# Optimization experiments

Hardware: AMD Instinct MI355X
Metric: run time of the kernel (lower is better)

The kernel has to match this reference:

```python
import jax, jax.numpy as jnp
import numpy as np
from jax import lax

N_EXPERTS = 16
TOP_K = 2
D_MODEL = 512
D_FF = 2048


def setup_inputs() -> dict:
    key = jax.random.key(0)
    ks = jax.random.split(key, 7)
    s_in = 1.0 / np.sqrt(D_MODEL)
    s_ff = 1.0 / np.sqrt(D_FF)
    x = jax.random.normal(ks[0], (2, 2048, D_MODEL), dtype=jnp.float32)
    router_w = jax.random.uniform(ks[1], (N_EXPERTS, D_MODEL), jnp.float32, -s_in, s_in)
    router_b = jax.random.uniform(ks[2], (N_EXPERTS,), jnp.float32, -s_in, s_in)
    w1 = jax.random.uniform(ks[3], (N_EXPERTS, D_FF, D_MODEL), jnp.float32, -s_in, s_in)
    b1 = jax.random.uniform(ks[4], (N_EXPERTS, D_FF), jnp.float32, -s_in, s_in)
    w2 = jax.random.uniform(ks[5], (N_EXPERTS, D_MODEL, D_FF), jnp.float32, -s_ff, s_ff)
    b2 = jax.random.uniform(ks[6], (N_EXPERTS, D_MODEL), jnp.float32, -s_ff, s_ff)
    return {"x": x, "router_w": router_w, "router_b": router_b,
            "w1": w1, "b1": b1, "w2": w2, "b2": b2}


def reference(x, router_w, router_b, w1, b1, w2, b2):
    B, S, D = x.shape
    xt = x.reshape(-1, D)                                   # [T, D]
    logits = xt @ router_w.T + router_b                     # [T, E]
    probs = jax.nn.softmax(logits, axis=-1)
    topk_p, topk_i = lax.top_k(probs, TOP_K)                # [T, K]
    # Dense gate matrix: gate[t, e] = topk prob if expert e selected else 0.
    # Weighting by gate reproduces the masked gather/scatter-add exactly.
    onehot = jax.nn.one_hot(topk_i, N_EXPERTS, dtype=probs.dtype)  # [T, K, E]
    gates = jnp.sum(onehot * topk_p[..., None], axis=1)     # [T, E]

    def expert_step(acc, packed):
        w1e, b1e, w2e, b2e, ge = packed                     # per-expert params + gate col [T]
        h = jax.nn.gelu(xt @ w1e.T + b1e, approximate=False)  # [T, D_FF]
        y = h @ w2e.T + b2e                                 # [T, D]
        return acc + y * ge[:, None], None

    out, _ = lax.scan(expert_step, jnp.zeros_like(xt),
                      (w1, b1, w2, b2, gates.T))
    return out.reshape(B, S, D)
```

## Files before the change

### kernel.cpp

```cpp
#include <hip/hip_runtime.h>
#include <stdint.h>

#define T_TOK 4096
#define DM    512
#define DFF   2048
#define NE    16
#define NSLOT (T_TOK * 2)
#define NW    (NE * DFF * DM)
#define MAXTILE 80
#define CONVB (2 * NW / 8 / 256)
#define ROUTB (T_TOK / 4)
#define KSPLIT 4

typedef __attribute__((ext_vector_type(8))) short  bf16x8;
typedef __attribute__((ext_vector_type(4))) float  f32x4;
typedef __attribute__((ext_vector_type(8))) unsigned short us8;

static __device__ __forceinline__ unsigned short f2bf(float f) {
    unsigned int u = __float_as_uint(f);
    u += 0x7FFFu + ((u >> 16) & 1u);
    return (unsigned short)(u >> 16);
}

static __device__ __forceinline__ void gload_lds16(const void* g, void* l) {
    __builtin_amdgcn_global_load_lds(
        (const __attribute__((address_space(1))) void*)g,
        (__attribute__((address_space(3))) void*)l, 16, 0, 0);
}

static __device__ __forceinline__ int xcd_chunk_logical(int bid, int total) {
    int k = bid & 7, seq = bid >> 3;
    int q = total >> 3, r = total & 7;
    int base = k * q + (k < r ? k : r);
    int len  = q + (k < r ? 1 : 0);
    return (seq < len) ? (base + seq) : total;
}

__global__ __launch_bounds__(256) void convert_router_kernel(
    const float* __restrict__ w1, const float* __restrict__ w2,
    unsigned short* __restrict__ w1b, unsigned short* __restrict__ w2b,
    const float* __restrict__ x, const float* __restrict__ rw,
    const float* __restrict__ rb, int* __restrict__ tok_e,
    float* __restrict__ tok_g, unsigned short* __restrict__ xb,
    const float* __restrict__ b2, float* __restrict__ out)
{
    __shared__ float rws[NE * DM];
    int tid = threadIdx.x;

    if (blockIdx.x >= ROUTB) {
        size_t i = ((size_t)(blockIdx.x - ROUTB) * 256 + tid) * 8;
        const float* src; unsigned short* dst;
        if (i < (size_t)NW) { src = w1 + i;        dst = w1b + i; }
        else                { src = w2 + (i - NW); dst = w2b + (i - NW); }
        f32x4 a = __builtin_nontemporal_load((const f32x4*)src);
        f32x4 b = __builtin_nontemporal_load((const f32x4*)(src + 4));
        us8 v;
        v[0] = f2bf(a.x); v[1] = f2bf(a.y); v[2] = f2bf(a.z); v[3] = f2bf(a.w);
        v[4] = f2bf(b.x); v[5] = f2bf(b.y); v[6] = f2bf(b.z); v[7] = f2bf(b.w);
        *(us8*)dst = v;
        return;
    }

    for (int i = 0; i < 8; ++i) {
        int idx = (tid + i * 256) * 4;
        *(f32x4*)&rws[idx] = *(const f32x4*)&rw[idx];
    }
    __syncthreads();

    int wid = tid >> 6, lane = tid & 63;
    int t = blockIdx.x * 4 + wid;

    float xv[8];
    const float* xp = x + (size_t)t * DM + lane * 8;
    *(f32x4*)&xv[0] = *(const f32x4*)xp;
    *(f32x4*)&xv[4] = *(const f32x4*)(xp + 4);

    us8 v;
    for (int i = 0; i < 8; ++i) v[i] = f2bf(xv[i]);
    *(us8*)&xb[(size_t)t * DM + lane * 8] = v;

    float acc[NE];
    for (int e = 0; e < NE; ++e) {
        const float* wp = &rws[e * DM + lane * 8];
        float a = 0.f;
        for (int i = 0; i < 8; ++i) a += xv[i] * wp[i];
        acc[e] = a;
    }
    for (int e = 0; e < NE; ++e) {
        float v2 = acc[e];
        for (int off = 32; off > 0; off >>= 1) v2 += __shfl_xor(v2, off);
        acc[e] = v2 + rb[e];
    }
    float m = acc[0];
    for (int e = 1; e < NE; ++e) m = fmaxf(m, acc[e]);
    float p[NE]; float s = 0.f;
    for (int e = 0; e < NE; ++e) { p[e] = expf(acc[e] - m); s += p[e]; }
    float inv = 1.f / s;
    int i0 = 0; float p0 = p[0];
    for (int e = 1; e < NE; ++e) if (p[e] > p0) { p0 = p[e]; i0 = e; }
    int i1 = (i0 == 0) ? 1 : 0; float p1 = p[i1];
    for (int e = 0; e < NE; ++e)
        if (e != i0 && p[e] > p1) { p1 = p[e]; i1 = e; }
    float g0 = p0 * inv, g1 = p1 * inv;
    if (lane == 0) {
        tok_e[t * 2]     = i0;  tok_e[t * 2 + 1] = i1;
        tok_g[t * 2]     = g0;
        tok_g[t * 2 + 1] = g1;
    }
    {
        int d = lane * 8;
        f32x4 c0a = *(const f32x4*)&b2[i0 * DM + d];
        f32x4 c0b = *(const f32x4*)&b2[i0 * DM + d + 4];
        f32x4 c1a = *(const f32x4*)&b2[i1 * DM + d];
        f32x4 c1b = *(const f32x4*)&b2[i1 * DM + d + 4];
        f32x4 oa, ob;
        for (int i = 0; i < 4; ++i) {
            oa[i] = g0 * c0a[i] + g1 * c1a[i];
            ob[i] = g0 * c0b[i] + g1 * c1b[i];
        }
        *(f32x4*)&out[(size_t)t * DM + d]     = oa;
        *(f32x4*)&out[(size_t)t * DM + d + 4] = ob;
    }
}

__global__ __launch_bounds__(1024) void compact_kernel(
    const int* __restrict__ tok_e, const float* __restrict__ tok_g,
    int* __restrict__ slot_token, float* __restrict__ slot_gate,
    int* __restrict__ eoff)
{
    __shared__ int wsum[16][NE];
    __shared__ int wbase[16][NE];
    __shared__ int ebl[NE];
    int tid = threadIdx.x;
    int wv = tid >> 6, lane = tid & 63;

    int ent[8];
    *(int4*)&ent[0] = *(const int4*)&tok_e[tid * 8];
    *(int4*)&ent[4] = *(const int4*)&tok_e[tid * 8 + 4];
    float gv[8];
    *(f32x4*)&gv[0] = *(const f32x4*)&tok_g[tid * 8];
    *(f32x4*)&gv[4] = *(const f32x4*)&tok_g[tid * 8 + 4];

    int cnt[NE], isc[NE];
#pragma unroll
    for (int e = 0; e < NE; ++e) {
        int c = 0;
#pragma unroll
        for (int i = 0; i < 8; ++i) c += (ent[i] == e) ? 1 : 0;
        int v = c;
#pragma unroll
        for (int off = 1; off < 64; off <<= 1) {
            int u = __shfl_up(v, off);
            if (lane >= off) v += u;
        }
        cnt[e] = c; isc[e] = v;
    }
    if (lane == 63) {
#pragma unroll
        for (int e = 0; e < NE; ++e) wsum[wv][e] = isc[e];
    }
    __syncthreads();
    if (wv == 0 && lane < NE) {
        int e = lane, s = 0;
#pragma unroll
        for (int w = 0; w < 16; ++w) { wbase[w][e] = s; s += wsum[w][e]; }
        int til = (s + 127) >> 7;
        int rs = s, rt = til;
#pragma unroll
        for (int off = 1; off < 16; off <<= 1) {
            int u1 = __shfl_up(rs, off);
            int u2 = __shfl_up(rt, off);
            if (lane >= off) { rs += u1; rt += u2; }
        }
        ebl[e] = rs - s;
        eoff[e] = rs - s;
        eoff[16 + e] = s;
        eoff[32 + e] = rt - til;
        if (e == NE - 1) eoff[48] = rt;
    }
    __syncthreads();
    int ofs[NE];
#pragma unroll
    for (int e = 0; e < NE; ++e)
        ofs[e] = ebl[e] + wbase[wv][e] + isc[e] - cnt[e];
#pragma unroll
    for (int i = 0; i < 8; ++i) {
        int ei = ent[i], s = 0;
#pragma unroll
        for (int e = 0; e < NE; ++e) if (ei == e) s = ofs[e];
        slot_token[s] = tid * 4 + (i >> 1);
        slot_gate[s]  = gv[i];
#pragma unroll
        for (int e = 0; e < NE; ++e) if (ei == e) ofs[e] = s + 1;
    }
}

__global__ __launch_bounds__(256) void gemm1_kernel(
    const unsigned short* __restrict__ xb, const unsigned short* __restrict__ w1b,
    const float* __restrict__ b1, const int* __restrict__ slot_token,
    const int* __restrict__ eoff, unsigned short* __restrict__ h)
{
    __shared__ unsigned short smem[16384];
    __shared__ int tokrow[128];
    __shared__ int meta[49];
    unsigned short* As = smem;
    unsigned short* Bs = smem + 8192;

    int tid = threadIdx.x;
    if (tid < 49) meta[tid] = eoff[tid];
    __syncthreads();

    int lg = xcd_chunk_logical(blockIdx.x, meta[48] * 16);
    int slot_idx = lg >> 4;
    if (slot_idx >= meta[48]) return;
    int nB = (lg & 15) * 128;
    int e = 0;
    while (e < NE - 1 && meta[32 + e + 1] <= slot_idx) ++e;
    int mt  = slot_idx - meta[32 + e];
    int off = meta[e], cnt = meta[16 + e];
    int slot0 = off + mt * 128;
    int valid = cnt - mt * 128; if (valid > 128) valid = 128;

    if (tid < 128) {
        int s = slot0 + tid; if (s > NSLOT - 1) s = NSLOT - 1;
        tokrow[tid] = slot_token[s];
    }
    __syncthreads();

    f32x4 acc[16];
    for (int i = 0; i < 16; ++i) acc[i] = (f32x4){0.f, 0.f, 0.f, 0.f};

    const unsigned short* wb = w1b + ((size_t)e * DFF + nB) * DM;
    int wid = tid >> 6, l = tid & 63;
    int wm = (wid & 1) * 64, wn = (wid >> 1) * 64;
    int q = l >> 4, c = l & 15;

    for (int kt = 0; kt < DM / 64; ++kt) {
        for (int j = 0; j < 4; ++j) {
            int u = (wid * 4 + j) * 64 + l;
            int row = u >> 3, sc = (u & 7) ^ (row & 7);
            gload_lds16(xb + (size_t)tokrow[row] * DM + kt * 64 + sc * 8, &As[u * 8]);
        }
        for (int j = 0; j < 4; ++j) {
            int u = (wid * 4 + j) * 64 + l;
            int row = u >> 3, sc = (u & 7) ^ (row & 7);
            gload_lds16(wb + (size_t)row * DM + kt * 64 + sc * 8, &Bs[u * 8]);
        }
        __syncthreads();
        for (int ks = 0; ks < 2; ++ks) {
            int sw = ((ks * 4 + q) ^ (c & 7)) * 8;
            bf16x8 af[4], bv[4];
            for (int i = 0; i < 4; ++i) af[i] = *(bf16x8*)&As[(wm + i * 16 + c) * 64 + sw];
            for (int j = 0; j < 4; ++j) bv[j] = *(bf16x8*)&Bs[(wn + j * 16 + c) * 64 + sw];
            for (int i = 0; i < 4; ++i)
                for (int j = 0; j < 4; ++j)
                    acc[i * 4 + j] = __builtin_amdgcn_mfma_f32_16x16x32_bf16(
                        af[i], bv[j], acc[i * 4 + j], 0, 0, 0);
        }
        __syncthreads();
    }

    float bias[4];
    for (int j = 0; j < 4; ++j) bias[j] = b1[e * DFF + nB + wn + j * 16 + c];
    unsigned short* bounce = smem;
    for (int ph = 0; ph < 2; ++ph) {
        __syncthreads();
        if ((wid & 1) == ph) {
            for (int i = 0; i < 4; ++i)
                for (int j = 0; j < 4; ++j) {
                    f32x4 a = acc[i * 4 + j];
                    for (int r = 0; r < 4; ++r) {
                        int rl = i * 16 + q * 4 + r;
                        float z = a[r] + bias[j];
                        float u2 = z * fmaf(0.0356774081f, z * z, 0.7978845608f);
                        float ex = __expf(2.0f * u2);
                        float th = 1.0f - 2.0f * __builtin_amdgcn_rcpf(ex + 1.0f);
                        float g = 0.5f * z * (1.0f + th);
                        bounce[rl * 136 + wn + j * 16 + c] = f2bf(g);
                    }
                }
        }
        __syncthreads();
        for (int it = 0; it < 4; ++it) {
            int u2 = it * 256 + tid;
            int row = u2 >> 4, ch = u2 & 15;
            int gr = ph * 64 + row;
            if (gr < valid)
                *(us8*)&h[(size_t)(slot0 + gr) * DFF + nB + ch * 8] =
                    *(us8*)&bounce[row * 136 + ch * 8];
        }
    }
}

__global__ __launch_bounds__(256) void gemm2_kernel(
    const unsigned short* __restrict__ h, const unsigned short* __restrict__ w2b,
    const int* __restrict__ eoff, const int* __restrict__ slot_token,
    const float* __restrict__ slot_gate, float* __restrict__ out)
{
    __shared__ unsigned short smem[16384];
    __shared__ int meta[49];
    __shared__ int tokrow[128];
    __shared__ float sgate[128];
    unsigned short* As = smem;
    unsigned short* Bs = smem + 8192;

    int tid = threadIdx.x;
    if (tid < 49) meta[tid] = eoff[tid];
    __syncthreads();

    int lg = xcd_chunk_logical(blockIdx.x, meta[48] * 16);
    int slot_idx = lg >> 4;
    if (slot_idx >= meta[48]) return;
    int nB = (lg & 3) * 128;
    int z  = (lg >> 2) & 3;
    int e = 0;
    while (e < NE - 1 && meta[32 + e + 1] <= slot_idx) ++e;
    int mt  = slot_idx - meta[32 + e];
    int off = meta[e], cnt = meta[16 + e];
    int slot0 = off + mt * 128;
    int valid = cnt - mt * 128; if (valid > 128) valid = 128;

    if (tid < 128) {
        int s = slot0 + tid; if (s > NSLOT - 1) s = NSLOT - 1;
        tokrow[tid] = slot_token[s];
        sgate[tid]  = slot_gate[s];
    }
    __syncthreads();

    f32x4 acc[16];
    for (int i = 0; i < 16; ++i) acc[i] = (f32x4){0.f, 0.f, 0.f, 0.f};

    const unsigned short* wb = w2b + ((size_t)e * DM + nB) * DFF
                             + (size_t)z * (DFF / KSPLIT);
    const unsigned short* hz = h + (size_t)z * (DFF / KSPLIT);
    int wid = tid >> 6, l = tid & 63;
    int wm = (wid & 1) * 64, wn = (wid >> 1) * 64;
    int q = l >> 4, c = l & 15;

    for (int kt = 0; kt < DFF / (64 * KSPLIT); ++kt) {
        for (int j = 0; j < 4; ++j) {
            int u = (wid * 4 + j) * 64 + l;
            int row = u >> 3, sc = (u & 7) ^ (row & 7);
            size_t s = slot0 + row; if (s > NSLOT - 1) s = NSLOT - 1;
            gload_lds16(hz + s * DFF + kt * 64 + sc * 8, &As[u * 8]);
        }
        for (int j = 0; j < 4; ++j) {
            int u = (wid * 4 + j) * 64 + l;
            int row = u >> 3, sc = (u & 7) ^ (row & 7);
            gload_lds16(wb + (size_t)row * DFF + kt * 64 + sc * 8, &Bs[u * 8]);
        }
        __syncthreads();
        for (int ks = 0; ks < 2; ++ks) {
            int sw = ((ks * 4 + q) ^ (c & 7)) * 8;
            bf16x8 af[4], bv[4];
            for (int i = 0; i < 4; ++i) af[i] = *(bf16x8*)&As[(wm + i * 16 + c) * 64 + sw];
            for (int j = 0; j < 4; ++j) bv[j] = *(bf16x8*)&Bs[(wn + j * 16 + c) * 64 + sw];
            for (int i = 0; i < 4; ++i)
                for (int j = 0; j < 4; ++j)
                    acc[i * 4 + j] = __builtin_amdgcn_mfma_f32_16x16x32_bf16(
                        af[i], bv[j], acc[i * 4 + j], 0, 0, 0);
        }
        __syncthreads();
    }

    for (int i = 0; i < 4; ++i)
        for (int j = 0; j < 4; ++j) {
            int n = nB + wn + j * 16 + c;
            for (int r = 0; r < 4; ++r) {
                int rl = wm + i * 16 + q * 4 + r;
                if (rl < valid)
                    atomicAdd(&out[(size_t)tokrow[rl] * DM + n],
                              sgate[rl] * acc[i * 4 + j][r]);
            }
        }
}

extern "C" void kernel_launch(void* const* d_in, const int* in_sizes, int n_in,
                              void* d_out, int out_size, void* d_ws, size_t ws_size,
                              hipStream_t stream) {
    const float* x  = (const float*)d_in[0];
    const float* rw = (const float*)d_in[1];
    const float* rb = (const float*)d_in[2];
    const float* w1 = (const float*)d_in[3];
    const float* b1 = (const float*)d_in[4];
    const float* w2 = (const float*)d_in[5];
    const float* b2 = (const float*)d_in[6];
    float* out = (float*)d_out;

    char* ws = (char*)d_ws;
    size_t o = 0;
    unsigned short* h   = (unsigned short*)(ws + o); o += (size_t)NSLOT * DFF * 2;
    unsigned short* w1b = (unsigned short*)(ws + o); o += (size_t)NW * 2;
    unsigned short* w2b = (unsigned short*)(ws + o); o += (size_t)NW * 2;
    unsigned short* xb  = (unsigned short*)(ws + o); o += (size_t)T_TOK * DM * 2;
    int*   tok_e      = (int*)(ws + o);   o += (size_t)NSLOT * 4;
    float* tok_g      = (float*)(ws + o); o += (size_t)NSLOT * 4;
    int*   slot_token = (int*)(ws + o);   o += (size_t)NSLOT * 4;
    float* slot_gate  = (float*)(ws + o); o += (size_t)NSLOT * 4;
    int*   eoff       = (int*)(ws + o);

    convert_router_kernel<<<ROUTB + CONVB, 256, 0, stream>>>(
        w1, w2, w1b, w2b, x, rw, rb, tok_e, tok_g, xb, b2, out);
    compact_kernel<<<1, 1024, 0, stream>>>(
        tok_e, tok_g, slot_token, slot_gate, eoff);
    gemm1_kernel<<<16 * MAXTILE, 256, 0, stream>>>(
        xb, w1b, b1, slot_token, eoff, h);
    gemm2_kernel<<<4 * MAXTILE * KSPLIT, 256, 0, stream>>>(
        h, w2b, eoff, slot_token, slot_gate, out);
}
```

Baseline: 304.2 us.

## Replace gemm2 atomic scatter with per-split slot buffers and a combine kernel

The second GEMM now writes plain, non-atomic partial outputs per slot into two K-split buffers, which reuse the w1 bf16 workspace after gemm1 finishes. A new combine kernel then gathers each token's two slots, adds both K-split partials and the expert bias, applies the gates, and writes the output once. KSPLIT drops from 4 to 2, so gemm2 launches fewer but longer blocks. This removes scattered float atomics and the bias pre-initialisation in the router, at the cost of an extra kernel launch and extra memory traffic for the intermediate y buffers.

```diff
diff --git a/kernel.cpp b/kernel.cpp
--- a/kernel.cpp
+++ b/kernel.cpp
@@ -6,11 +6,11 @@
 #define DFF   2048
 #define NE    16
 #define NSLOT (T_TOK * 2)
-#define NW    (NE * DFF * DM)
+#define NW    (16 * 2048 * 512)
 #define MAXTILE 80
 #define CONVB (2 * NW / 8 / 256)
 #define ROUTB (T_TOK / 4)
-#define KSPLIT 4
+#define KSPLIT 2
 
 typedef __attribute__((ext_vector_type(8))) short  bf16x8;
 typedef __attribute__((ext_vector_type(4))) float  f32x4;
@@ -41,8 +41,7 @@
     unsigned short* __restrict__ w1b, unsigned short* __restrict__ w2b,
     const float* __restrict__ x, const float* __restrict__ rw,
     const float* __restrict__ rb, int* __restrict__ tok_e,
-    float* __restrict__ tok_g, unsigned short* __restrict__ xb,
-    const float* __restrict__ b2, float* __restrict__ out)
+    float* __restrict__ tok_g, unsigned short* __restrict__ xb)
 {
     __shared__ float rws[NE * DM];
     int tid = threadIdx.x;
@@ -101,32 +100,16 @@
     int i1 = (i0 == 0) ? 1 : 0; float p1 = p[i1];
     for (int e = 0; e < NE; ++e)
         if (e != i0 && p[e] > p1) { p1 = p[e]; i1 = e; }
-    float g0 = p0 * inv, g1 = p1 * inv;
     if (lane == 0) {
         tok_e[t * 2]     = i0;  tok_e[t * 2 + 1] = i1;
-        tok_g[t * 2]     = g0;
-        tok_g[t * 2 + 1] = g1;
-    }
-    {
-        int d = lane * 8;
-        f32x4 c0a = *(const f32x4*)&b2[i0 * DM + d];
-        f32x4 c0b = *(const f32x4*)&b2[i0 * DM + d + 4];
-        f32x4 c1a = *(const f32x4*)&b2[i1 * DM + d];
-        f32x4 c1b = *(const f32x4*)&b2[i1 * DM + d + 4];
-        f32x4 oa, ob;
-        for (int i = 0; i < 4; ++i) {
-            oa[i] = g0 * c0a[i] + g1 * c1a[i];
-            ob[i] = g0 * c0b[i] + g1 * c1b[i];
-        }
-        *(f32x4*)&out[(size_t)t * DM + d]     = oa;
-        *(f32x4*)&out[(size_t)t * DM + d + 4] = ob;
+        tok_g[t * 2]     = p0 * inv;
+        tok_g[t * 2 + 1] = p1 * inv;
     }
 }
 
 __global__ __launch_bounds__(1024) void compact_kernel(
-    const int* __restrict__ tok_e, const float* __restrict__ tok_g,
-    int* __restrict__ slot_token, float* __restrict__ slot_gate,
-    int* __restrict__ eoff)
+    const int* __restrict__ tok_e, int* __restrict__ slot_token,
+    int* __restrict__ tok_slot, int* __restrict__ eoff)
 {
     __shared__ int wsum[16][NE];
     __shared__ int wbase[16][NE];
@@ -137,9 +120,6 @@
     int ent[8];
     *(int4*)&ent[0] = *(const int4*)&tok_e[tid * 8];
     *(int4*)&ent[4] = *(const int4*)&tok_e[tid * 8 + 4];
-    float gv[8];
-    *(f32x4*)&gv[0] = *(const f32x4*)&tok_g[tid * 8];
-    *(f32x4*)&gv[4] = *(const f32x4*)&tok_g[tid * 8 + 4];
 
     int cnt[NE], isc[NE];
 #pragma unroll
@@ -189,7 +169,7 @@
 #pragma unroll
         for (int e = 0; e < NE; ++e) if (ei == e) s = ofs[e];
         slot_token[s] = tid * 4 + (i >> 1);
-        slot_gate[s]  = gv[i];
+        tok_slot[tid * 8 + i] = s;
 #pragma unroll
         for (int e = 0; e < NE; ++e) if (ei == e) ofs[e] = s + 1;
     }
@@ -294,13 +274,10 @@
 
 __global__ __launch_bounds__(256) void gemm2_kernel(
     const unsigned short* __restrict__ h, const unsigned short* __restrict__ w2b,
-    const int* __restrict__ eoff, const int* __restrict__ slot_token,
-    const float* __restrict__ slot_gate, float* __restrict__ out)
+    const int* __restrict__ eoff, float* __restrict__ y)
 {
     __shared__ unsigned short smem[16384];
     __shared__ int meta[49];
-    __shared__ int tokrow[128];
-    __shared__ float sgate[128];
     unsigned short* As = smem;
     unsigned short* Bs = smem + 8192;
 
@@ -308,24 +285,17 @@
     if (tid < 49) meta[tid] = eoff[tid];
     __syncthreads();
 
-    int lg = xcd_chunk_logical(blockIdx.x, meta[48] * 16);
-    int slot_idx = lg >> 4;
+    int lg = xcd_chunk_logical(blockIdx.x, meta[48] * 8);
+    int slot_idx = lg >> 3;
     if (slot_idx >= meta[48]) return;
     int nB = (lg & 3) * 128;
-    int z  = (lg >> 2) & 3;
+    int z  = (lg >> 2) & 1;
     int e = 0;
     while (e < NE - 1 && meta[32 + e + 1] <= slot_idx) ++e;
     int mt  = slot_idx - meta[32 + e];
     int off = meta[e], cnt = meta[16 + e];
     int slot0 = off + mt * 128;
     int valid = cnt - mt * 128; if (valid > 128) valid = 128;
-
-    if (tid < 128) {
-        int s = slot0 + tid; if (s > NSLOT - 1) s = NSLOT - 1;
-        tokrow[tid] = slot_token[s];
-        sgate[tid]  = slot_gate[s];
-    }
-    __syncthreads();
 
     f32x4 acc[16];
     for (int i = 0; i < 16; ++i) acc[i] = (f32x4){0.f, 0.f, 0.f, 0.f};
@@ -363,16 +333,40 @@
         __syncthreads();
     }
 
+    float* yz = y + (size_t)z * NSLOT * DM;
     for (int i = 0; i < 4; ++i)
         for (int j = 0; j < 4; ++j) {
             int n = nB + wn + j * 16 + c;
             for (int r = 0; r < 4; ++r) {
                 int rl = wm + i * 16 + q * 4 + r;
                 if (rl < valid)
-                    atomicAdd(&out[(size_t)tokrow[rl] * DM + n],
-                              sgate[rl] * acc[i * 4 + j][r]);
+                    yz[(size_t)(slot0 + rl) * DM + n] = acc[i * 4 + j][r];
             }
         }
+}
+
+__global__ __launch_bounds__(256) void combine_kernel(
+    const float* __restrict__ y, const float* __restrict__ b2,
+    const int* __restrict__ tok_slot, const float* __restrict__ tok_g,
+    const int* __restrict__ tok_e, float* __restrict__ out)
+{
+    int tid = threadIdx.x;
+    int t = blockIdx.x * 2 + (tid >> 7);
+    int d = (tid & 127) * 4;
+    int s0 = tok_slot[t * 2], s1 = tok_slot[t * 2 + 1];
+    float g0 = tok_g[t * 2], g1 = tok_g[t * 2 + 1];
+    int e0 = tok_e[t * 2], e1 = tok_e[t * 2 + 1];
+    const float* yB = y + (size_t)NSLOT * DM;
+    f32x4 y0a = *(const f32x4*)&y [(size_t)s0 * DM + d];
+    f32x4 y0b = *(const f32x4*)&yB[(size_t)s0 * DM + d];
+    f32x4 y1a = *(const f32x4*)&y [(size_t)s1 * DM + d];
+    f32x4 y1b = *(const f32x4*)&yB[(size_t)s1 * DM + d];
+    f32x4 c0 = *(const f32x4*)&b2[e0 * DM + d];
+    f32x4 c1 = *(const f32x4*)&b2[e1 * DM + d];
+    f32x4 o;
+    for (int i = 0; i < 4; ++i)
+        o[i] = g0 * (y0a[i] + y0b[i] + c0[i]) + g1 * (y1a[i] + y1b[i] + c1[i]);
+    *(f32x4*)&out[(size_t)t * DM + d] = o;
 }
 
 extern "C" void kernel_launch(void* const* d_in, const int* in_sizes, int n_in,
@@ -395,16 +389,19 @@
     unsigned short* xb  = (unsigned short*)(ws + o); o += (size_t)T_TOK * DM * 2;
     int*   tok_e      = (int*)(ws + o);   o += (size_t)NSLOT * 4;
     float* tok_g      = (float*)(ws + o); o += (size_t)NSLOT * 4;
+    int*   tok_slot   = (int*)(ws + o);   o += (size_t)NSLOT * 4;
     int*   slot_token = (int*)(ws + o);   o += (size_t)NSLOT * 4;
-    float* slot_gate  = (float*)(ws + o); o += (size_t)NSLOT * 4;
     int*   eoff       = (int*)(ws + o);
+    float* y = (float*)w1b;
 
     convert_router_kernel<<<ROUTB + CONVB, 256, 0, stream>>>(
-        w1, w2, w1b, w2b, x, rw, rb, tok_e, tok_g, xb, b2, out);
+        w1, w2, w1b, w2b, x, rw, rb, tok_e, tok_g, xb);
     compact_kernel<<<1, 1024, 0, stream>>>(
-        tok_e, tok_g, slot_token, slot_gate, eoff);
+        tok_e, slot_token, tok_slot, eoff);
     gemm1_kernel<<<16 * MAXTILE, 256, 0, stream>>>(
         xb, w1b, b1, slot_token, eoff, h);
-    gemm2_kernel<<<4 * MAXTILE * KSPLIT, 256, 0, stream>>>(
-        h, w2b, eoff, slot_token, slot_gate, out);
-}
+    gemm2_kernel<<<8 * MAXTILE, 256, 0, stream>>>(
+        h, w2b, eoff, y);
+    combine_kernel<<<T_TOK / 2, 256, 0, stream>>>(
+        y, b2, tok_slot, tok_g, tok_e, out);
+}
```

Measured after the change: 274.1 us. -9.9%, faster.
